# Optimization experiments

Hardware: AMD Instinct MI355X
Metric: run time of the kernel (lower is better)

The kernel has to match this reference:

```python
import jax, jax.numpy as jnp
import numpy as np

B, T, I, H, NG = 50, 512, 1024, 512, 2048  # batch, seq, input, hidden(=reduced), 4*H
O = 2


def setup_inputs() -> dict:
    key = jax.random.key(0)
    ks = jax.random.split(key, 16)
    s = 0.05  # weight scale to keep gates/tanh in a sane range
    return {
        "input": jax.random.normal(ks[0], (B, T, I), jnp.float32),
        "pca_W": jax.random.normal(ks[1], (H, I), jnp.float32) * s,
        "pca_b": jax.random.normal(ks[2], (H,), jnp.float32) * s,
        "W_ih0": jax.random.normal(ks[3], (NG, H), jnp.float32) * s,
        "W_hh0": jax.random.normal(ks[4], (NG, H), jnp.float32) * s,
        "b0": jax.random.normal(ks[5], (NG,), jnp.float32) * s,
        "W_ih1": jax.random.normal(ks[6], (NG, H), jnp.float32) * s,
        "W_hh1": jax.random.normal(ks[7], (NG, H), jnp.float32) * s,
        "b1": jax.random.normal(ks[8], (NG,), jnp.float32) * s,
        "h0": jax.random.normal(ks[9], (2, B, H), jnp.float32),
        "c0": jax.random.normal(ks[10], (2, B, H), jnp.float32),
        "lin1_W": jax.random.normal(ks[11], (10, H), jnp.float32) * s,
        "lin1_b": jax.random.normal(ks[12], (10,), jnp.float32) * s,
        "lin2_W": jax.random.normal(ks[13], (O, 10), jnp.float32) * s,
        "lin2_b": jax.random.normal(ks[14], (O,), jnp.float32) * s,
    }


def _lstm_layer(x, h0, c0, W_ih, W_hh, b):
    # x: [B,T,H_in]; precompute input-to-gate projections once (PyTorch gate order i,f,g,o)
    xg = jnp.einsum('bti,gi->btg', x, W_ih) + b  # [B,T,4H]

    def step(carry, xt):
        h, c = carry
        g = xt + h @ W_hh.T  # [B,4H]
        i_, f_, g_, o_ = jnp.split(g, 4, axis=-1)
        c = jax.nn.sigmoid(f_) * c + jax.nn.sigmoid(i_) * jnp.tanh(g_)
        h = jax.nn.sigmoid(o_) * jnp.tanh(c)
        return (h, c), h

    _, hs = jax.lax.scan(step, (h0, c0), jnp.swapaxes(xg, 0, 1))  # hs: [T,B,H]
    return jnp.swapaxes(hs, 0, 1)  # [B,T,H]


def reference(input, pca_W, pca_b, W_ih0, W_hh0, b0, W_ih1, W_hh1, b1,
              h0, c0, lin1_W, lin1_b, lin2_W, lin2_b):
    x = input @ pca_W.T + pca_b                      # pca_linear: [B,T,H]
    x = _lstm_layer(x, h0[0], c0[0], W_ih0, W_hh0, b0)
    x = _lstm_layer(x, h0[1], c0[1], W_ih1, W_hh1, b1)
    last = x[:, -1, :]                               # out[:, -1, :]
    out = jnp.tanh(last @ lin1_W.T + lin1_b)         # tanh(linear)
    return out @ lin2_W.T + lin2_b                   # linear2: [B,O]
```

## Files before the change

### kernel.cpp

```cpp
#include <hip/hip_runtime.h>
#include <math.h>

#define B_  50
#define T_  512
#define I_  1024
#define H_  512
#define NG_ 2048
#define NBLK 256
#define FLS  32

typedef __attribute__((ext_vector_type(8))) short short8;
typedef __attribute__((ext_vector_type(4))) float f32x4;
typedef unsigned short ushort_t;
typedef unsigned long long ull_t;

__device__ __forceinline__ float sigmf(float x) {
    return 1.0f / (1.0f + __expf(-x));
}
__device__ __forceinline__ float tanh_fast(float x) {
    float ax = fabsf(x);
    float e  = __expf(-2.0f * ax);
    float t  = (1.0f - e) / (1.0f + e);
    return copysignf(t, x);
}
__device__ __forceinline__ ushort_t bf16_rne(float x) {
    unsigned u = __float_as_uint(x);
    unsigned r = u + 0x7fffu + ((u >> 16) & 1u);
    return (ushort_t)(r >> 16);
}
__device__ __forceinline__ float bf16_tof(ushort_t h) {
    return __uint_as_float(((unsigned)h) << 16);
}

__global__ __launch_bounds__(256) void gemm_bias_mfma(
    const float* __restrict__ A, const float* __restrict__ W,
    const float* __restrict__ bias, float* __restrict__ C,
    int M, int N, int K, int tmode) {
    __shared__ ushort_t Ah[128 * 40];
    __shared__ ushort_t Al[128 * 40];
    __shared__ ushort_t Wh[128 * 40];
    __shared__ ushort_t Wl[128 * 40];
    const int tid = threadIdx.x;
    const int m0 = blockIdx.y * 128, n0 = blockIdx.x * 128;
    const int w = tid >> 6, L = tid & 63;
    const int wm = (w & 1) * 64, wn = (w >> 1) * 64;
    const int rr = tid >> 1, kh = (tid & 1) << 4;

    f32x4 acc[4][4];
#pragma unroll
    for (int i = 0; i < 4; ++i)
#pragma unroll
        for (int j = 0; j < 4; ++j) acc[i][j] = (f32x4){0.f, 0.f, 0.f, 0.f};

    for (int k0 = 0; k0 < K; k0 += 32) {
        float4 av[4], wv[4];
        const float* ap = A + (size_t)(m0 + rr) * K + k0 + kh;
        const float* wp = W + (size_t)(n0 + rr) * K + k0 + kh;
#pragma unroll
        for (int e = 0; e < 4; ++e) {
            av[e] = *(const float4*)(ap + 4 * e);
            wv[e] = *(const float4*)(wp + 4 * e);
        }
        __syncthreads();
        union { ushort_t s[16]; ull_t u[4]; } ha, la, hw, lw;
#pragma unroll
        for (int e = 0; e < 4; ++e) {
            float as[4] = {av[e].x, av[e].y, av[e].z, av[e].w};
            float ws[4] = {wv[e].x, wv[e].y, wv[e].z, wv[e].w};
#pragma unroll
            for (int f = 0; f < 4; ++f) {
                ushort_t hi = bf16_rne(as[f]);
                ha.s[e * 4 + f] = hi;
                la.s[e * 4 + f] = bf16_rne(as[f] - bf16_tof(hi));
                hi = bf16_rne(ws[f]);
                hw.s[e * 4 + f] = hi;
                lw.s[e * 4 + f] = bf16_rne(ws[f] - bf16_tof(hi));
            }
        }
        {
            ull_t* d0 = (ull_t*)&Ah[rr * 40 + kh];
            ull_t* d1 = (ull_t*)&Al[rr * 40 + kh];
            ull_t* d2 = (ull_t*)&Wh[rr * 40 + kh];
            ull_t* d3 = (ull_t*)&Wl[rr * 40 + kh];
#pragma unroll
            for (int e = 0; e < 4; ++e) {
                d0[e] = ha.u[e]; d1[e] = la.u[e];
                d2[e] = hw.u[e]; d3[e] = lw.u[e];
            }
        }
        __syncthreads();
        const int ko = (L >> 4) * 8;
        short8 ahf[4], alf[4], whf[4], wlf[4];
#pragma unroll
        for (int i = 0; i < 4; ++i) {
            ahf[i] = *(const short8*)&Ah[(wm + i * 16 + (L & 15)) * 40 + ko];
            alf[i] = *(const short8*)&Al[(wm + i * 16 + (L & 15)) * 40 + ko];
            whf[i] = *(const short8*)&Wh[(wn + i * 16 + (L & 15)) * 40 + ko];
            wlf[i] = *(const short8*)&Wl[(wn + i * 16 + (L & 15)) * 40 + ko];
        }
#pragma unroll
        for (int i = 0; i < 4; ++i)
#pragma unroll
            for (int j = 0; j < 4; ++j) {
                acc[i][j] = __builtin_amdgcn_mfma_f32_16x16x32_bf16(ahf[i], whf[j], acc[i][j], 0, 0, 0);
                acc[i][j] = __builtin_amdgcn_mfma_f32_16x16x32_bf16(alf[i], whf[j], acc[i][j], 0, 0, 0);
                acc[i][j] = __builtin_amdgcn_mfma_f32_16x16x32_bf16(ahf[i], wlf[j], acc[i][j], 0, 0, 0);
            }
    }

#pragma unroll
    for (int j = 0; j < 4; ++j) {
        int col = n0 + wn + j * 16 + (L & 15);
        float bv = bias[col];
#pragma unroll
        for (int i = 0; i < 4; ++i) {
#pragma unroll
            for (int r = 0; r < 4; ++r) {
                int row = m0 + wm + i * 16 + (L >> 4) * 4 + r;
                size_t crow = tmode ? ((size_t)(row & (T_ - 1)) * B_ + (row >> 9))
                                    : (size_t)row;
                C[crow * N + col] = acc[i][j][r] + bv;
            }
        }
    }
}

__global__ __launch_bounds__(256) void init_hfrag(
    const float* __restrict__ h0, ushort_t* __restrict__ hf) {
    const int g = blockIdx.x, tid = threadIdx.x;
    const int bat0 = (g < 2) ? 7 * g : 14 + 6 * (g - 2);
    const int cnt  = (g < 2) ? 7 : 6;
    ushort_t* og = hf + (size_t)g * 8192;
    for (int i = tid; i < 8192; i += 256) {
        int jj = i & 7, cl = (i >> 3) & 31, ks = (i >> 8) & 15, hl = i >> 12;
        int m = cl & 7, oct = cl >> 3;
        int j = ks * 32 + oct * 8 + jj;
        float x = 0.0f;
        if (m < cnt) x = h0[(size_t)(bat0 + m) * H_ + j];
        ushort_t hi = bf16_rne(x);
        og[i] = hl ? bf16_rne(x - bf16_tof(hi)) : hi;
    }
}

__global__ __launch_bounds__(256, 1) void lstm_fused(
    const float* __restrict__ xg,
    ushort_t* __restrict__ hf0A, ushort_t* __restrict__ hf0B,
    ushort_t* __restrict__ hf1A, ushort_t* __restrict__ hf1B,
    const float* __restrict__ c0,
    const float* __restrict__ W_hh0,
    const float* __restrict__ W_hh1,
    const float* __restrict__ W_ih1,
    const float* __restrict__ b1,
    float* __restrict__ hplain,
    int* __restrict__ flags) {
    __shared__ __align__(16) ushort_t hfL0[16384];
    __shared__ __align__(16) ushort_t hfL1[16384];
    __shared__ float d0b[2][4 * 4 * 8 * 16];
    __shared__ float d1b[2][4 * 4 * 8 * 16];
    __shared__ short8 wlo[4 * 4 * 4 * 64];
    const int tid = threadIdx.x, bid = blockIdx.x;
    const int g = bid >> 5, mB = bid & 31;
    const int j0 = mB * 16;
    const int bat0 = (g < 2) ? 7 * g : 14 + 6 * (g - 2);
    const int cnt  = (g < 2) ? 7 : 6;
    const int w = tid >> 6, L = tid & 63;

    {
        ull_t* u0 = (ull_t*)hfL0;
        ull_t* u1 = (ull_t*)hfL1;
        for (int i = tid; i < 4096; i += 256)
            if ((((i >> 1) & 63) & 15) >= 8) { u0[i] = 0ULL; u1[i] = 0ULL; }
    }

    short8 Bhh0h[4][4], Bhh0l[4][4], Bhh1h[4][4], Bhh1l[4][4], Bih1h[4][4];
    {
        const int n = L & 15, oct = L >> 4;
#pragma unroll
        for (int q = 0; q < 4; ++q) {
            const size_t row = (size_t)(q * H_ + j0 + n) * H_;
#pragma unroll
            for (int kk = 0; kk < 4; ++kk) {
                int kbase = (w * 4 + kk) * 32 + oct * 8;
                {
                    float4 f0 = *(const float4*)(W_hh0 + row + kbase);
                    float4 f1 = *(const float4*)(W_hh0 + row + kbase + 4);
                    float xs[8] = {f0.x, f0.y, f0.z, f0.w, f1.x, f1.y, f1.z, f1.w};
                    union { ushort_t s[8]; short8 v; } uh, ul;
#pragma unroll
                    for (int e = 0; e < 8; ++e) {
                        ushort_t hi = bf16_rne(xs[e]);
                        uh.s[e] = hi; ul.s[e] = bf16_rne(xs[e] - bf16_tof(hi));
                    }
                    Bhh0h[q][kk] = uh.v; Bhh0l[q][kk] = ul.v;
                }
                {
                    float4 f0 = *(const float4*)(W_hh1 + row + kbase);
                    float4 f1 = *(const float4*)(W_hh1 + row + kbase + 4);
                    float xs[8] = {f0.x, f0.y, f0.z, f0.w, f1.x, f1.y, f1.z, f1.w};
                    union { ushort_t s[8]; short8 v; } uh, ul;
#pragma unroll
                    for (int e = 0; e < 8; ++e) {
                        ushort_t hi = bf16_rne(xs[e]);
                        uh.s[e] = hi; ul.s[e] = bf16_rne(xs[e] - bf16_tof(hi));
                    }
                    Bhh1h[q][kk] = uh.v; Bhh1l[q][kk] = ul.v;
                }
                {
                    float4 f0 = *(const float4*)(W_ih1 + row + kbase);
                    float4 f1 = *(const float4*)(W_ih1 + row + kbase + 4);
                    float xs[8] = {f0.x, f0.y, f0.z, f0.w, f1.x, f1.y, f1.z, f1.w};
                    union { ushort_t s[8]; short8 v; } uh, ul;
#pragma unroll
                    for (int e = 0; e < 8; ++e) {
                        ushort_t hi = bf16_rne(xs[e]);
                        uh.s[e] = hi; ul.s[e] = bf16_rne(xs[e] - bf16_tof(hi));
                    }
                    Bih1h[q][kk] = uh.v;
                    wlo[((w * 4 + q) * 4 + kk) * 64 + L] = ul.v;
                }
            }
        }
    }

    const int gm0 = tid >> 3, jlp0 = (tid & 7) * 2;
    const bool gok0 = (tid < 56) && (gm0 < cnt);
    const int gb0 = (bat0 + gm0 < B_) ? bat0 + gm0 : B_ - 1;
    float c0a = 0.f, c0b = 0.f;
    if (gok0) {
        c0a = c0[(size_t)gb0 * H_ + j0 + jlp0];
        c0b = c0[(size_t)gb0 * H_ + j0 + jlp0 + 1];
    }
    float2 xr[4];
    if (tid < 56) {
#pragma unroll
        for (int q = 0; q < 4; ++q)
            xr[q] = *(const float2*)(xg + (size_t)gb0 * NG_ + q * H_ + j0 + jlp0);
    }
    const int u1 = tid - 64;
    const int gm1 = u1 >> 3, jlp1 = (u1 & 7) * 2;
    const bool gok1 = (tid >= 64) && (tid < 120) && (gm1 < cnt);
    const int gb1 = (gok1 && bat0 + gm1 < B_) ? bat0 + gm1 : B_ - 1;
    float c1a = 0.f, c1b = 0.f;
    float2 b1r[4];
    if (gok1) {
        c1a = c0[(size_t)(B_ + gb1) * H_ + j0 + jlp1];
        c1b = c0[(size_t)(B_ + gb1) * H_ + j0 + jlp1 + 1];
#pragma unroll
        for (int q = 0; q < 4; ++q)
            b1r[q] = *(const float2*)(b1 + q * H_ + j0 + jlp1);
    }

    __syncthreads();

    const short8* ap0 = (const short8*)hfL0;
    const short8* ap1 = (const short8*)hfL1;
    const f32x4 vzero = {0.f, 0.f, 0.f, 0.f};

    const int* pollf = flags + (size_t)(g * 32 + 8 * w + (L & 7)) * FLS + ((L >> 3) & 1);

    for (int s = 0; s <= T_; ++s) {
        const ushort_t* r0 = (s & 1) ? hf0A : hf0B;
        ushort_t*       w0 = (s & 1) ? hf0B : hf0A;
        const ushort_t* r1 = (s & 1) ? hf1B : hf1A;
        ushort_t*       w1 = (s & 1) ? hf1A : hf1B;
        float* dw0 = d0b[s & 1];
        float* dw1 = d1b[s & 1];

        {
            for (;;) {
                int v = (L < 16)
                        ? __hip_atomic_load(pollf, __ATOMIC_RELAXED, __HIP_MEMORY_SCOPE_AGENT)
                        : s;
                if (__all(v >= s)) break;
                __builtin_amdgcn_s_sleep(2);
            }
        }

        {
            const ull_t* s0 = (const ull_t*)(r0 + (size_t)g * 8192);
            const ull_t* s1 = (const ull_t*)(r1 + (size_t)g * 8192);
            ull_t* l0 = (ull_t*)hfL0;
            ull_t* l1 = (ull_t*)hfL1;
            ull_t v0[8], v1[8];
#pragma unroll
            for (int hl = 0; hl < 2; ++hl)
#pragma unroll
                for (int i = 0; i < 4; ++i) {
                    int u = hl * 1024 + w * 256 + i * 64 + L;
                    v0[hl * 4 + i] = __hip_atomic_load(s0 + u, __ATOMIC_RELAXED,
                                                       __HIP_MEMORY_SCOPE_AGENT);
                    v1[hl * 4 + i] = __hip_atomic_load(s1 + u, __ATOMIC_RELAXED,
                                                       __HIP_MEMORY_SCOPE_AGENT);
                }
#pragma unroll
            for (int hl = 0; hl < 2; ++hl)
#pragma unroll
                for (int i = 0; i < 4; ++i) {
                    int u = hl * 1024 + w * 256 + i * 64 + L;
                    int jjh = u & 1, cl = (u >> 1) & 31, ks = (u >> 6) & 15;
                    int el = (cl & 7) + 16 * (cl >> 3);
                    int di = ((hl * 16 + ks) * 64 + el) * 2 + jjh;
                    l0[di] = v0[hl * 4 + i];
                    l1[di] = v1[hl * 4 + i];
                }
        }

        if (s < T_) {
            f32x4 acc[4];
#pragma unroll
            for (int q = 0; q < 4; ++q) acc[q] = vzero;
#pragma unroll
            for (int kk = 0; kk < 4; ++kk) {
                int ksp = w * 4 + kk;
                short8 Ahi = ap0[ksp * 64 + L];
                short8 Alo = ap0[1024 + ksp * 64 + L];
#pragma unroll
                for (int q = 0; q < 4; ++q) {
                    acc[q] = __builtin_amdgcn_mfma_f32_16x16x32_bf16(Ahi, Bhh0h[q][kk], acc[q], 0, 0, 0);
                    acc[q] = __builtin_amdgcn_mfma_f32_16x16x32_bf16(Alo, Bhh0h[q][kk], acc[q], 0, 0, 0);
                    acc[q] = __builtin_amdgcn_mfma_f32_16x16x32_bf16(Ahi, Bhh0l[q][kk], acc[q], 0, 0, 0);
                }
            }
#pragma unroll
            for (int q = 0; q < 4; ++q)
#pragma unroll
                for (int r = 0; r < 4; ++r) {
                    int m = (L >> 4) * 4 + r;
                    if (m < 8) dw0[((w * 4 + q) * 8 + m) * 16 + (L & 15)] = acc[q][r];
                }
        }
        if (s >= 1) {
            f32x4 acc[4];
#pragma unroll
            for (int q = 0; q < 4; ++q) acc[q] = vzero;
#pragma unroll
            for (int kk = 0; kk < 4; ++kk) {
                int ksp = w * 4 + kk;
                short8 A0h = ap0[ksp * 64 + L];
                short8 A0l = ap0[1024 + ksp * 64 + L];
                short8 A1h = ap1[ksp * 64 + L];
                short8 A1l = ap1[1024 + ksp * 64 + L];
#pragma unroll
                for (int q = 0; q < 4; ++q) {
                    short8 Wl = wlo[((w * 4 + q) * 4 + kk) * 64 + L];
                    acc[q] = __builtin_amdgcn_mfma_f32_16x16x32_bf16(A0h, Bih1h[q][kk], acc[q], 0, 0, 0);
                    acc[q] = __builtin_amdgcn_mfma_f32_16x16x32_bf16(A0l, Bih1h[q][kk], acc[q], 0, 0, 0);
                    acc[q] = __builtin_amdgcn_mfma_f32_16x16x32_bf16(A0h, Wl, acc[q], 0, 0, 0);
                    acc[q] = __builtin_amdgcn_mfma_f32_16x16x32_bf16(A1h, Bhh1h[q][kk], acc[q], 0, 0, 0);
                    acc[q] = __builtin_amdgcn_mfma_f32_16x16x32_bf16(A1l, Bhh1h[q][kk], acc[q], 0, 0, 0);
                    acc[q] = __builtin_amdgcn_mfma_f32_16x16x32_bf16(A1h, Bhh1l[q][kk], acc[q], 0, 0, 0);
                }
            }
#pragma unroll
            for (int q = 0; q < 4; ++q)
#pragma unroll
                for (int r = 0; r < 4; ++r) {
                    int m = (L >> 4) * 4 + r;
                    if (m < 8) dw1[((w * 4 + q) * 8 + m) * 16 + (L & 15)] = acc[q][r];
                }
        }
        __syncthreads();

        if (s < T_) {
            if (gok0) {
                float ga[4], gb[4];
#pragma unroll
                for (int q = 0; q < 4; ++q) {
                    float sx = 0.f, sy = 0.f;
#pragma unroll
                    for (int ww = 0; ww < 4; ++ww) {
                        const float2 p = *(const float2*)&dw0[((ww * 4 + q) * 8 + gm0) * 16 + jlp0];
                        sx += p.x; sy += p.y;
                    }
                    ga[q] = sx + xr[q].x;
                    gb[q] = sy + xr[q].y;
                }
                float cna = sigmf(ga[1]) * c0a + sigmf(ga[0]) * tanh_fast(ga[2]);
                float hna = sigmf(ga[3]) * tanh_fast(cna);
                float cnb = sigmf(gb[1]) * c0b + sigmf(gb[0]) * tanh_fast(gb[2]);
                float hnb = sigmf(gb[3]) * tanh_fast(cnb);
                c0a = cna; c0b = cnb;
                ushort_t hia = bf16_rne(hna), hib = bf16_rne(hnb);
                ushort_t loa = bf16_rne(hna - bf16_tof(hia));
                ushort_t lob = bf16_rne(hnb - bf16_tof(hib));
                int jA = j0 + jlp0;
                int cl = gm0 + 8 * ((jA >> 3) & 3);
                int ks = jA >> 5, jj = jA & 7;
                ushort_t* og = w0 + (size_t)g * 8192;
                unsigned hv = (unsigned)hia | ((unsigned)hib << 16);
                unsigned lv = (unsigned)loa | ((unsigned)lob << 16);
                __hip_atomic_store((unsigned*)(og + (ks * 256 + cl * 8 + jj)), hv,
                                   __ATOMIC_RELAXED, __HIP_MEMORY_SCOPE_AGENT);
                __hip_atomic_store((unsigned*)(og + (4096 + ks * 256 + cl * 8 + jj)), lv,
                                   __ATOMIC_RELAXED, __HIP_MEMORY_SCOPE_AGENT);
            }
        }
        if (tid == 0) {
            asm volatile("s_waitcnt vmcnt(0)" ::: "memory");
            __hip_atomic_store(flags + (size_t)bid * FLS + 0, s + 1,
                               __ATOMIC_RELAXED, __HIP_MEMORY_SCOPE_AGENT);
        }
        if (tid < 56 && s + 1 < T_) {
#pragma unroll
            for (int q = 0; q < 4; ++q)
                xr[q] = *(const float2*)(xg + ((size_t)(s + 1) * B_ + gb0) * NG_ + q * H_ + j0 + jlp0);
        }

        if (s >= 1 && gok1) {
            float ga[4], gb[4];
#pragma unroll
            for (int q = 0; q < 4; ++q) {
                float sx = 0.f, sy = 0.f;
#pragma unroll
                for (int ww = 0; ww < 4; ++ww) {
                    const float2 p = *(const float2*)&dw1[((ww * 4 + q) * 8 + gm1) * 16 + jlp1];
                    sx += p.x; sy += p.y;
                }
                ga[q] = sx + b1r[q].x;
                gb[q] = sy + b1r[q].y;
            }
            float cna = sigmf(ga[1]) * c1a + sigmf(ga[0]) * tanh_fast(ga[2]);
            float hna = sigmf(ga[3]) * tanh_fast(cna);
            float cnb = sigmf(gb[1]) * c1b + sigmf(gb[0]) * tanh_fast(gb[2]);
            float hnb = sigmf(gb[3]) * tanh_fast(cnb);
            c1a = cna; c1b = cnb;
            ushort_t hia = bf16_rne(hna), hib = bf16_rne(hnb);
            ushort_t loa = bf16_rne(hna - bf16_tof(hia));
            ushort_t lob = bf16_rne(hnb - bf16_tof(hib));
            int jA = j0 + jlp1;
            int cl = gm1 + 8 * ((jA >> 3) & 3);
            int ks = jA >> 5, jj = jA & 7;
            ushort_t* og = w1 + (size_t)g * 8192;
            unsigned hv = (unsigned)hia | ((unsigned)hib << 16);
            unsigned lv = (unsigned)loa | ((unsigned)lob << 16);
            __hip_atomic_store((unsigned*)(og + (ks * 256 + cl * 8 + jj)), hv,
                               __ATOMIC_RELAXED, __HIP_MEMORY_SCOPE_AGENT);
            __hip_atomic_store((unsigned*)(og + (4096 + ks * 256 + cl * 8 + jj)), lv,
                               __ATOMIC_RELAXED, __HIP_MEMORY_SCOPE_AGENT);
            if (s == T_) *(float2*)(hplain + (size_t)gb1 * H_ + jA) = make_float2(hna, hnb);
        }
        if (tid == 64) {
            asm volatile("s_waitcnt vmcnt(0)" ::: "memory");
            __hip_atomic_store(flags + (size_t)bid * FLS + 1, s + 1,
                               __ATOMIC_RELAXED, __HIP_MEMORY_SCOPE_AGENT);
        }
    }
}

__global__ __launch_bounds__(512) void head(
    const float* __restrict__ hT, const float* __restrict__ lin1_W,
    const float* __restrict__ lin1_b, const float* __restrict__ lin2_W,
    const float* __restrict__ lin2_b, float* __restrict__ out) {
    __shared__ float zs[B_][10];
    int tid = threadIdx.x;
    if (tid < B_ * 10) {
        int b = tid / 10, u = tid % 10;
        float acc = lin1_b[u];
        for (int j = 0; j < H_; j += 4) {
            float4 hv = *(const float4*)&hT[(size_t)b * H_ + j];
            float4 wv = *(const float4*)&lin1_W[(size_t)u * H_ + j];
            acc = fmaf(hv.x, wv.x, acc);
            acc = fmaf(hv.y, wv.y, acc);
            acc = fmaf(hv.z, wv.z, acc);
            acc = fmaf(hv.w, wv.w, acc);
        }
        zs[b][u] = tanh_fast(acc);
    }
    __syncthreads();
    if (tid < B_ * 2) {
        int b = tid >> 1, o = tid & 1;
        float acc = lin2_b[o];
#pragma unroll
        for (int u = 0; u < 10; ++u)
            acc = fmaf(zs[b][u], lin2_W[o * 10 + u], acc);
        out[b * 2 + o] = acc;
    }
}

extern "C" void kernel_launch(void* const* d_in, const int* in_sizes, int n_in,
                              void* d_out, int out_size, void* d_ws, size_t ws_size,
                              hipStream_t stream) {
    const float* input  = (const float*)d_in[0];
    const float* pca_W  = (const float*)d_in[1];
    const float* pca_b  = (const float*)d_in[2];
    const float* W_ih0  = (const float*)d_in[3];
    const float* W_hh0  = (const float*)d_in[4];
    const float* b0     = (const float*)d_in[5];
    const float* W_ih1  = (const float*)d_in[6];
    const float* W_hh1  = (const float*)d_in[7];
    const float* b1     = (const float*)d_in[8];
    const float* h0     = (const float*)d_in[9];
    const float* c0     = (const float*)d_in[10];
    const float* lin1_W = (const float*)d_in[11];
    const float* lin1_b = (const float*)d_in[12];
    const float* lin2_W = (const float*)d_in[13];
    const float* lin2_b = (const float*)d_in[14];
    float* out = (float*)d_out;

    float* ws = (float*)d_ws;
    size_t off = 0;
    float* xg     = ws + off; off += (size_t)B_ * T_ * NG_;
    float* xbuf   = ws + off; off += (size_t)B_ * T_ * H_;
    float* hplain = ws + off; off += B_ * H_;
    ushort_t* hf0A = (ushort_t*)(ws + off); off += 32768;
    ushort_t* hf0B = (ushort_t*)(ws + off); off += 32768;
    ushort_t* hf1A = (ushort_t*)(ws + off); off += 32768;
    ushort_t* hf1B = (ushort_t*)(ws + off); off += 32768;
    int* flg = (int*)(ws + off); off += NBLK * FLS;

    const int M = B_ * T_;

    hipMemsetAsync(flg, 0, NBLK * FLS * sizeof(int), stream);

    init_hfrag<<<8, 256, 0, stream>>>(h0, hf0B);
    init_hfrag<<<8, 256, 0, stream>>>(h0 + B_ * H_, hf1B);

    {
        dim3 g(H_ / 128, M / 128);
        gemm_bias_mfma<<<g, 256, 0, stream>>>(input, pca_W, pca_b, xbuf, M, H_, I_, 0);
    }
    {
        dim3 g(NG_ / 128, M / 128);
        gemm_bias_mfma<<<g, 256, 0, stream>>>(xbuf, W_ih0, b0, xg, M, NG_, H_, 1);
    }
    lstm_fused<<<NBLK, 256, 0, stream>>>(xg, hf0A, hf0B, hf1A, hf1B, c0,
                                         W_hh0, W_hh1, W_ih1, b1, hplain, flg);
    head<<<1, 512, 0, stream>>>(hplain, lin1_W, lin1_b, lin2_W, lin2_b, out);
}
```

Measured before the change: 3.308 ms.

## Interleave LDS staging of hidden state with per-k MFMA for both layers

Restructures the per-step loop so the global-to-LDS scatter of the exchanged hidden state is interleaved with the MFMA accumulation for each k-slice. Both layers' accumulations now run in one fused loop that shares the layer-0 A fragments. The spin-wait sleep is also removed so polling for the step flag reacts faster. The aim is to overlap load latency with matrix math and cut the barrier-to-barrier critical path. The cost is more live accumulator registers and more memory traffic from busier polling.

```diff
diff --git a/kernel.cpp b/kernel.cpp
--- a/kernel.cpp
+++ b/kernel.cpp
@@ -272,7 +272,6 @@
                         ? __hip_atomic_load(pollf, __ATOMIC_RELAXED, __HIP_MEMORY_SCOPE_AGENT)
                         : s;
                 if (__all(v >= s)) break;
-                __builtin_amdgcn_s_sleep(2);
             }
         }
 
@@ -281,83 +280,75 @@
             const ull_t* s1 = (const ull_t*)(r1 + (size_t)g * 8192);
             ull_t* l0 = (ull_t*)hfL0;
             ull_t* l1 = (ull_t*)hfL1;
-            ull_t v0[8], v1[8];
-#pragma unroll
-            for (int hl = 0; hl < 2; ++hl)
-#pragma unroll
-                for (int i = 0; i < 4; ++i) {
+            ull_t v0[4][2], v1[4][2];
+#pragma unroll
+            for (int i = 0; i < 4; ++i)
+#pragma unroll
+                for (int hl = 0; hl < 2; ++hl) {
                     int u = hl * 1024 + w * 256 + i * 64 + L;
-                    v0[hl * 4 + i] = __hip_atomic_load(s0 + u, __ATOMIC_RELAXED,
-                                                       __HIP_MEMORY_SCOPE_AGENT);
-                    v1[hl * 4 + i] = __hip_atomic_load(s1 + u, __ATOMIC_RELAXED,
-                                                       __HIP_MEMORY_SCOPE_AGENT);
-                }
-#pragma unroll
-            for (int hl = 0; hl < 2; ++hl)
-#pragma unroll
-                for (int i = 0; i < 4; ++i) {
+                    v0[i][hl] = __hip_atomic_load(s0 + u, __ATOMIC_RELAXED,
+                                                  __HIP_MEMORY_SCOPE_AGENT);
+                    v1[i][hl] = __hip_atomic_load(s1 + u, __ATOMIC_RELAXED,
+                                                  __HIP_MEMORY_SCOPE_AGENT);
+                }
+            f32x4 acc0[4], acc1[4];
+#pragma unroll
+            for (int q = 0; q < 4; ++q) { acc0[q] = vzero; acc1[q] = vzero; }
+#pragma unroll
+            for (int i = 0; i < 4; ++i) {
+#pragma unroll
+                for (int hl = 0; hl < 2; ++hl) {
                     int u = hl * 1024 + w * 256 + i * 64 + L;
                     int jjh = u & 1, cl = (u >> 1) & 31, ks = (u >> 6) & 15;
                     int el = (cl & 7) + 16 * (cl >> 3);
                     int di = ((hl * 16 + ks) * 64 + el) * 2 + jjh;
-                    l0[di] = v0[hl * 4 + i];
-                    l1[di] = v1[hl * 4 + i];
-                }
-        }
-
-        if (s < T_) {
-            f32x4 acc[4];
-#pragma unroll
-            for (int q = 0; q < 4; ++q) acc[q] = vzero;
-#pragma unroll
-            for (int kk = 0; kk < 4; ++kk) {
-                int ksp = w * 4 + kk;
+                    l0[di] = v0[i][hl];
+                    l1[di] = v1[i][hl];
+                }
+                const int ksp = w * 4 + i;
                 short8 Ahi = ap0[ksp * 64 + L];
                 short8 Alo = ap0[1024 + ksp * 64 + L];
-#pragma unroll
-                for (int q = 0; q < 4; ++q) {
-                    acc[q] = __builtin_amdgcn_mfma_f32_16x16x32_bf16(Ahi, Bhh0h[q][kk], acc[q], 0, 0, 0);
-                    acc[q] = __builtin_amdgcn_mfma_f32_16x16x32_bf16(Alo, Bhh0h[q][kk], acc[q], 0, 0, 0);
-                    acc[q] = __builtin_amdgcn_mfma_f32_16x16x32_bf16(Ahi, Bhh0l[q][kk], acc[q], 0, 0, 0);
-                }
-            }
-#pragma unroll
-            for (int q = 0; q < 4; ++q)
-#pragma unroll
-                for (int r = 0; r < 4; ++r) {
-                    int m = (L >> 4) * 4 + r;
-                    if (m < 8) dw0[((w * 4 + q) * 8 + m) * 16 + (L & 15)] = acc[q][r];
-                }
-        }
-        if (s >= 1) {
-            f32x4 acc[4];
-#pragma unroll
-            for (int q = 0; q < 4; ++q) acc[q] = vzero;
-#pragma unroll
-            for (int kk = 0; kk < 4; ++kk) {
-                int ksp = w * 4 + kk;
-                short8 A0h = ap0[ksp * 64 + L];
-                short8 A0l = ap0[1024 + ksp * 64 + L];
-                short8 A1h = ap1[ksp * 64 + L];
-                short8 A1l = ap1[1024 + ksp * 64 + L];
-#pragma unroll
-                for (int q = 0; q < 4; ++q) {
-                    short8 Wl = wlo[((w * 4 + q) * 4 + kk) * 64 + L];
-                    acc[q] = __builtin_amdgcn_mfma_f32_16x16x32_bf16(A0h, Bih1h[q][kk], acc[q], 0, 0, 0);
-                    acc[q] = __builtin_amdgcn_mfma_f32_16x16x32_bf16(A0l, Bih1h[q][kk], acc[q], 0, 0, 0);
-                    acc[q] = __builtin_amdgcn_mfma_f32_16x16x32_bf16(A0h, Wl, acc[q], 0, 0, 0);
-                    acc[q] = __builtin_amdgcn_mfma_f32_16x16x32_bf16(A1h, Bhh1h[q][kk], acc[q], 0, 0, 0);
-                    acc[q] = __builtin_amdgcn_mfma_f32_16x16x32_bf16(A1l, Bhh1h[q][kk], acc[q], 0, 0, 0);
-                    acc[q] = __builtin_amdgcn_mfma_f32_16x16x32_bf16(A1h, Bhh1l[q][kk], acc[q], 0, 0, 0);
-                }
-            }
-#pragma unroll
-            for (int q = 0; q < 4; ++q)
-#pragma unroll
-                for (int r = 0; r < 4; ++r) {
-                    int m = (L >> 4) * 4 + r;
-                    if (m < 8) dw1[((w * 4 + q) * 8 + m) * 16 + (L & 15)] = acc[q][r];
-                }
+                if (s < T_) {
+#pragma unroll
+                    for (int q = 0; q < 4; ++q) {
+                        acc0[q] = __builtin_amdgcn_mfma_f32_16x16x32_bf16(Ahi, Bhh0h[q][i], acc0[q], 0, 0, 0);
+                        acc0[q] = __builtin_amdgcn_mfma_f32_16x16x32_bf16(Alo, Bhh0h[q][i], acc0[q], 0, 0, 0);
+                        acc0[q] = __builtin_amdgcn_mfma_f32_16x16x32_bf16(Ahi, Bhh0l[q][i], acc0[q], 0, 0, 0);
+                    }
+                }
+                if (s >= 1) {
+                    short8 A1h = ap1[ksp * 64 + L];
+                    short8 A1l = ap1[1024 + ksp * 64 + L];
+#pragma unroll
+                    for (int q = 0; q < 4; ++q) {
+                        short8 Wl = wlo[((w * 4 + q) * 4 + i) * 64 + L];
+                        acc1[q] = __builtin_amdgcn_mfma_f32_16x16x32_bf16(Ahi, Bih1h[q][i], acc1[q], 0, 0, 0);
+                        acc1[q] = __builtin_amdgcn_mfma_f32_16x16x32_bf16(Alo, Bih1h[q][i], acc1[q], 0, 0, 0);
+                        acc1[q] = __builtin_amdgcn_mfma_f32_16x16x32_bf16(Ahi, Wl, acc1[q], 0, 0, 0);
+                        acc1[q] = __builtin_amdgcn_mfma_f32_16x16x32_bf16(A1h, Bhh1h[q][i], acc1[q], 0, 0, 0);
+                        acc1[q] = __builtin_amdgcn_mfma_f32_16x16x32_bf16(A1l, Bhh1h[q][i], acc1[q], 0, 0, 0);
+                        acc1[q] = __builtin_amdgcn_mfma_f32_16x16x32_bf16(A1h, Bhh1l[q][i], acc1[q], 0, 0, 0);
+                    }
+                }
+            }
+            if (s < T_) {
+#pragma unroll
+                for (int q = 0; q < 4; ++q)
+#pragma unroll
+                    for (int r = 0; r < 4; ++r) {
+                        int m = (L >> 4) * 4 + r;
+                        if (m < 8) dw0[((w * 4 + q) * 8 + m) * 16 + (L & 15)] = acc0[q][r];
+                    }
+            }
+            if (s >= 1) {
+#pragma unroll
+                for (int q = 0; q < 4; ++q)
+#pragma unroll
+                    for (int r = 0; r < 4; ++r) {
+                        int m = (L >> 4) * 4 + r;
+                        if (m < 8) dw1[((w * 4 + q) * 8 + m) * 16 + (L & 15)] = acc1[q][r];
+                    }
+            }
         }
         __syncthreads();
 
```

Measured after the change: 3.643 ms. 10.1% more time.
